# Kernel tuning notes

Measured on AMD Instinct MI355X. Metric: run time of the kernel, lower is better.

Reference implementation:

```python
import jax, jax.numpy as jnp
import numpy as np

B, D, K, M1, M2 = 256, 128, 32, 64, 32   # batch, n_nodes, K copies, dims[1], dims[2]
H1, H2, L = 128, 64, 32                   # pivae_dims


def setup_inputs() -> dict:
    key = jax.random.key(0)
    ks = iter(jax.random.split(key, 32))

    def rn(shape, scale):
        return jax.random.normal(next(ks), shape, dtype=jnp.float32) * scale

    x = jax.random.normal(next(ks), (B, D), dtype=jnp.float32)

    # per-node fc1 weights: [D, M1, D]; bounds force nonneg with zero diag column
    W1_pos = jnp.abs(rn((D, M1, D), 1.0 / np.sqrt(D)))
    W1_neg = jnp.abs(rn((D, M1, D), 1.0 / np.sqrt(D)))
    eye = jnp.eye(D, dtype=jnp.float32)[:, None, :]   # zero out W[j,:,j]
    W1_pos = W1_pos * (1.0 - eye)
    W1_neg = W1_neg * (1.0 - eye)
    b1_pos = rn((D, M1), 0.02)
    b1_neg = rn((D, M1), 0.02)

    # LocallyConnected stacks: weight [K, m_in, m_out]
    lc1_w = rn((K, M1, M2), 1.0 / np.sqrt(M1)); lc1_b = rn((K, M2), 0.02)
    lc2_w = rn((K, M2, 1), 1.0 / np.sqrt(M2));  lc2_b = rn((K, 1), 0.02)

    # per-sample beta Linear(k,1): weights [B, K], bias [B]
    beta_w = rn((B, K), 1.0 / np.sqrt(K)); beta_b = rn((B,), 0.02)

    # VAE params (encoder -> mu/logvar -> decoder), stored as (in,out) matrices
    enc1_w = rn((K, H1), 1.0 / np.sqrt(K));  enc1_b = jnp.zeros((H1,), jnp.float32)
    enc2_w = rn((H1, H2), 1.0 / np.sqrt(H1)); enc2_b = jnp.zeros((H2,), jnp.float32)
    mu_w = rn((H2, L), 1.0 / np.sqrt(H2));    mu_b = jnp.zeros((L,), jnp.float32)
    lv_w = rn((H2, L), 1.0 / np.sqrt(H2));    lv_b = jnp.zeros((L,), jnp.float32)
    dec1_w = rn((L, H2), 1.0 / np.sqrt(L));   dec1_b = jnp.zeros((H2,), jnp.float32)
    dec2_w = rn((H2, H1), 1.0 / np.sqrt(H2)); dec2_b = jnp.zeros((H1,), jnp.float32)
    dec3_w = rn((H1, K), 1.0 / np.sqrt(H1));  dec3_b = jnp.zeros((K,), jnp.float32)

    eps = jax.random.normal(next(ks), (B, L), dtype=jnp.float32)  # reparam noise

    return dict(x=x, W1_pos=W1_pos, W1_neg=W1_neg, b1_pos=b1_pos, b1_neg=b1_neg,
                lc1_w=lc1_w, lc1_b=lc1_b, lc2_w=lc2_w, lc2_b=lc2_b,
                beta_w=beta_w, beta_b=beta_b,
                enc1_w=enc1_w, enc1_b=enc1_b, enc2_w=enc2_w, enc2_b=enc2_b,
                mu_w=mu_w, mu_b=mu_b, lv_w=lv_w, lv_b=lv_b,
                dec1_w=dec1_w, dec1_b=dec1_b, dec2_w=dec2_w, dec2_b=dec2_b,
                dec3_w=dec3_w, dec3_b=dec3_b, eps=eps)


def reference(x, W1_pos, W1_neg, b1_pos, b1_neg, lc1_w, lc1_b, lc2_w, lc2_b,
              beta_w, beta_b, enc1_w, enc1_b, enc2_w, enc2_b, mu_w, mu_b,
              lv_w, lv_b, dec1_w, dec1_b, dec2_w, dec2_b, dec3_w, dec3_b, eps):
    b, d = x.shape
    k = lc1_w.shape[0]

    # fused per-node fc1: (pos - neg) applied to x with column j zeroed, all j at once
    W1 = W1_pos - W1_neg                      # [D, M1, D]
    b1 = b1_pos - b1_neg                      # [D, M1]
    full = jnp.einsum('bi,jhi->bjh', x, W1)   # as if no column were zeroed
    diagW = jnp.einsum('jhj->jh', W1)         # [D, M1] column-j weight of node j
    phi = full - x[:, :, None] * diagW[None] + b1[None]   # [B, D, M1]

    # expand to K copies, run sigmoid + LocallyConnected stack
    h = jnp.broadcast_to(phi[:, :, None, :], (b, d, k, phi.shape[-1]))
    h = jnp.einsum('bdkm,kmn->bdkn', jax.nn.sigmoid(h), lc1_w) + lc1_b   # [B,D,K,M2]
    h = jnp.einsum('bdkm,kmn->bdkn', jax.nn.sigmoid(h), lc2_w) + lc2_b   # [B,D,K,1]
    last_phi_x = h[..., 0]                    # [B, D, K]

    # per-sample beta projection (batched over B)
    y1 = jnp.einsum('bdk,bk->bd', last_phi_x, beta_w) + beta_b[:, None]

    # VAE on the stacked beta weights [B, K]
    e = jax.nn.relu(beta_w @ enc1_w + enc1_b)
    e = jax.nn.relu(e @ enc2_w + enc2_b)
    mu = e @ mu_w + mu_b
    logvar = e @ lv_w + lv_b
    z = mu + eps * jnp.exp(0.5 * logvar)
    dh = jax.nn.relu(z @ dec1_w + dec1_b)
    dh = jax.nn.relu(dh @ dec2_w + dec2_b)
    recon = dh @ dec3_w + dec3_b              # [B, K]

    y2 = jnp.einsum('bdk,bk->bd', last_phi_x, recon) + beta_b[:, None]
    return (y1, y2, mu, logvar)
```

## Files before the change

kernel.cpp:

```cpp
#include <hip/hip_runtime.h>
#include <stdint.h>

#define BB 256
#define DD 128
#define KK 32
#define MM1 64
#define MM2 32

typedef __attribute__((ext_vector_type(8))) short bf16x8;
typedef __attribute__((ext_vector_type(4))) float f32x4;

#define LOG2E 1.44269504088896f


__device__ __forceinline__ short f2b(float f) {
  uint32_t u = __builtin_bit_cast(uint32_t, f);
  u += 0x7FFFu + ((u >> 16) & 1u);
  return (short)(u >> 16);
}
__device__ __forceinline__ float sigm_pre(float acc, float cpre) {
  return __builtin_amdgcn_rcpf(
      1.0f + __builtin_amdgcn_exp2f(fmaf(acc, -LOG2E, cpre)));
}

__global__ __launch_bounds__(256) void prep_kernel(
    const float* __restrict__ x, const float* __restrict__ W1p,
    const float* __restrict__ W1n, const float* __restrict__ b1p,
    const float* __restrict__ b1n, const float* __restrict__ lc1w,
    const float* __restrict__ lc1b, const float* __restrict__ lc2b,
    const float* __restrict__ betaw, char* __restrict__ ws)
{
  const int tid = blockIdx.x * 256 + threadIdx.x;

  {
    float4 a = ((const float4*)W1p)[tid];
    float4 b = ((const float4*)W1n)[tid];
    short4 s;
    s.x = f2b(a.x - b.x); s.y = f2b(a.y - b.y);
    s.z = f2b(a.z - b.z); s.w = f2b(a.w - b.w);
    ((short4*)(ws + 303104))[tid] = s;
  }
  if (tid < 8192) {
    float4 v = ((const float4*)x)[tid];
    short4 s;
    s.x = f2b(v.x); s.y = f2b(v.y); s.z = f2b(v.z); s.w = f2b(v.w);
    ((short4*)(ws + 65536))[tid] = s;
  }
  if (tid < 65536) {
    int k = tid >> 11, n = (tid >> 6) & 31, m = tid & 63;
    ((short*)(ws + 131072))[tid] = f2b(lc1w[k * 2048 + m * 32 + n]);
  }
  if (tid < 8192) {
    ((float*)(ws + 32768))[tid] = betaw[(tid & 255) * 32 + (tid >> 8)];
  }
  if (tid < 1024) {
    ((float*)(ws + 262144))[tid] = -lc1b[tid] * LOG2E;
  }
  if (tid < 32) { ((float*)(ws + 266240))[tid] = 0.25f * lc2b[tid]; }
  if (tid < 8192) {
    ((float*)(ws + 270336))[tid] = -(b1p[tid] - b1n[tid]) * LOG2E;
  }
}

__global__ __launch_bounds__(128) void vae_kernel(
    const float* __restrict__ betaw,
    const float* __restrict__ enc1w, const float* __restrict__ enc1b,
    const float* __restrict__ enc2w, const float* __restrict__ enc2b,
    const float* __restrict__ muw,  const float* __restrict__ mub,
    const float* __restrict__ lvw,  const float* __restrict__ lvb,
    const float* __restrict__ dec1w, const float* __restrict__ dec1b,
    const float* __restrict__ dec2w, const float* __restrict__ dec2b,
    const float* __restrict__ dec3w, const float* __restrict__ dec3b,
    const float* __restrict__ eps,
    float* __restrict__ mu_out, float* __restrict__ lv_out,
    float* __restrict__ reconT)
{
  const int b = blockIdx.x, t = threadIdx.x;
  __shared__ float bw[KK], e1[128], e2[64], zz[32], d1s[64], d2s[128];
  if (t < KK) bw[t] = betaw[b * KK + t];
  __syncthreads();
  {
    float a0 = enc1b[t], a1 = 0.f;
    #pragma unroll
    for (int k = 0; k < KK; k += 2) {
      a0 = fmaf(bw[k], enc1w[k * 128 + t], a0);
      a1 = fmaf(bw[k + 1], enc1w[(k + 1) * 128 + t], a1);
    }
    e1[t] = fmaxf(a0 + a1, 0.f);
  }
  __syncthreads();
  if (t < 64) {
    float a0 = enc2b[t], a1 = 0.f, a2 = 0.f, a3 = 0.f;
    #pragma unroll 8
    for (int h = 0; h < 128; h += 4) {
      a0 = fmaf(e1[h], enc2w[h * 64 + t], a0);
      a1 = fmaf(e1[h + 1], enc2w[(h + 1) * 64 + t], a1);
      a2 = fmaf(e1[h + 2], enc2w[(h + 2) * 64 + t], a2);
      a3 = fmaf(e1[h + 3], enc2w[(h + 3) * 64 + t], a3);
    }
    e2[t] = fmaxf((a0 + a1) + (a2 + a3), 0.f);
  }
  __syncthreads();
  if (t < 32) {
    float m0 = mub[t], m1 = 0.f, l0 = lvb[t], l1 = 0.f;
    #pragma unroll 8
    for (int h = 0; h < 64; h += 2) {
      float ea = e2[h], eb = e2[h + 1];
      m0 = fmaf(ea, muw[h * 32 + t], m0);
      m1 = fmaf(eb, muw[(h + 1) * 32 + t], m1);
      l0 = fmaf(ea, lvw[h * 32 + t], l0);
      l1 = fmaf(eb, lvw[(h + 1) * 32 + t], l1);
    }
    float m = m0 + m1, l = l0 + l1;
    mu_out[b * 32 + t] = m;
    lv_out[b * 32 + t] = l;
    zz[t] = fmaf(eps[b * 32 + t], __expf(0.5f * l), m);
  }
  __syncthreads();
  if (t < 64) {
    float a0 = dec1b[t], a1 = 0.f;
    #pragma unroll
    for (int l = 0; l < 32; l += 2) {
      a0 = fmaf(zz[l], dec1w[l * 64 + t], a0);
      a1 = fmaf(zz[l + 1], dec1w[(l + 1) * 64 + t], a1);
    }
    d1s[t] = fmaxf(a0 + a1, 0.f);
  }
  __syncthreads();
  {
    float a0 = dec2b[t], a1 = 0.f, a2 = 0.f, a3 = 0.f;
    #pragma unroll 8
    for (int h = 0; h < 64; h += 4) {
      a0 = fmaf(d1s[h], dec2w[h * 128 + t], a0);
      a1 = fmaf(d1s[h + 1], dec2w[(h + 1) * 128 + t], a1);
      a2 = fmaf(d1s[h + 2], dec2w[(h + 2) * 128 + t], a2);
      a3 = fmaf(d1s[h + 3], dec2w[(h + 3) * 128 + t], a3);
    }
    d2s[t] = fmaxf((a0 + a1) + (a2 + a3), 0.f);
  }
  __syncthreads();
  if (t < 32) {
    float a0 = dec3b[t], a1 = 0.f, a2 = 0.f, a3 = 0.f;
    #pragma unroll 8
    for (int h = 0; h < 128; h += 4) {
      a0 = fmaf(d2s[h], dec3w[h * 32 + t], a0);
      a1 = fmaf(d2s[h + 1], dec3w[(h + 1) * 32 + t], a1);
      a2 = fmaf(d2s[h + 2], dec3w[(h + 2) * 32 + t], a2);
      a3 = fmaf(d2s[h + 3], dec3w[(h + 3) * 32 + t], a3);
    }
    reconT[t * BB + b] = (a0 + a1) + (a2 + a3);
  }
}

__global__ __launch_bounds__(256) void main_kernel(
    const float* __restrict__ lc2w, const float* __restrict__ betab,
    const char* __restrict__ ws, float* __restrict__ out)
{
  const int bx = blockIdx.x;
  const int d = bx >> 3;
  const int bg = bx & 7;
  const int tid = threadIdx.x;
  const int wave = tid >> 6, lane = tid & 63;
  const int g = lane >> 4, l15 = lane & 15;
  const int gb0 = bg * 32 + l15, gb1 = gb0 + 16;

  const short* __restrict__ xbf   = (const short*)(ws + 65536);
  const short* __restrict__ lc1T  = (const short*)(ws + 131072);
  const float* __restrict__ lc1bs = (const float*)(ws + 262144);
  const float* __restrict__ lc2bq = (const float*)(ws + 266240);
  const float* __restrict__ b1s   = (const float*)(ws + 270336) + d * MM1;
  const short* __restrict__ w1bf  = (const short*)(ws + 303104) + d * (MM1 * DD);
  const float* __restrict__ betaT = (const float*)(ws + 32768);
  const float* __restrict__ recT  = (const float*)(ws + 0);

  __shared__ short sS[32 * 64];
  __shared__ float yred[4][64];

  {
    bf16x8 wbv[4];
    const int m = wave * 16 + l15;
    #pragma unroll
    for (int ks = 0; ks < 4; ++ks)
      wbv[ks] = *(const bf16x8*)(w1bf + m * DD + ks * 32 + g * 8);
    const float cpre = b1s[m];
    #pragma unroll
    for (int rt = 0; rt < 2; ++rt) {
      f32x4 acc = {0.f, 0.f, 0.f, 0.f};
      #pragma unroll
      for (int ks = 0; ks < 4; ++ks) {
        bf16x8 xa = *(const bf16x8*)(xbf + (bg * 32 + rt * 16 + l15) * DD +
                                     ks * 32 + g * 8);
        acc = __builtin_amdgcn_mfma_f32_16x16x32_bf16(xa, wbv[ks], acc, 0, 0, 0);
      }
      #pragma unroll
      for (int r = 0; r < 4; ++r) {
        const int bl = rt * 16 + g * 4 + r;
        float s = sigm_pre(acc[r], cpre);
        sS[bl * 64 + ((m & ~7) ^ ((bl & 7) << 3)) + (m & 7)] = f2b(s);
      }
    }
  }
  __syncthreads();

  const bf16x8 sa0 = *(const bf16x8*)&sS[l15 * 64 + ((g * 8) ^ ((l15 & 7) << 3))];
  const bf16x8 sa1 = *(const bf16x8*)&sS[l15 * 64 + ((32 + g * 8) ^ ((l15 & 7) << 3))];
  const bf16x8 sa2 = *(const bf16x8*)&sS[(16 + l15) * 64 + ((g * 8) ^ ((l15 & 7) << 3))];
  const bf16x8 sa3 = *(const bf16x8*)&sS[(16 + l15) * 64 + ((32 + g * 8) ^ ((l15 & 7) << 3))];

  float y1a = 0.f, y2a = 0.f, y1b = 0.f, y2b = 0.f;
  bf16x8 A0a, A1a, A2a, A3a, A0b, A1b, A2b, A3b;

#define PREFA(kk, S) { \
    const short* ap = lc1T + (kk) * 2048 + l15 * 64 + g * 8; \
    A0##S = *(const bf16x8*)(ap); \
    A1##S = *(const bf16x8*)(ap + 32); \
    A2##S = *(const bf16x8*)(ap + 1024); \
    A3##S = *(const bf16x8*)(ap + 1056); }

#define COMPUTE(kk, S) { \
    f32x4 acc00 = {0,0,0,0}, acc01 = {0,0,0,0}; \
    f32x4 acc10 = {0,0,0,0}, acc11 = {0,0,0,0}; \
    acc00 = __builtin_amdgcn_mfma_f32_16x16x32_bf16(A0##S, sa0, acc00, 0, 0, 0); \
    acc00 = __builtin_amdgcn_mfma_f32_16x16x32_bf16(A1##S, sa1, acc00, 0, 0, 0); \
    acc01 = __builtin_amdgcn_mfma_f32_16x16x32_bf16(A0##S, sa2, acc01, 0, 0, 0); \
    acc01 = __builtin_amdgcn_mfma_f32_16x16x32_bf16(A1##S, sa3, acc01, 0, 0, 0); \
    acc10 = __builtin_amdgcn_mfma_f32_16x16x32_bf16(A2##S, sa0, acc10, 0, 0, 0); \
    acc10 = __builtin_amdgcn_mfma_f32_16x16x32_bf16(A3##S, sa1, acc10, 0, 0, 0); \
    acc11 = __builtin_amdgcn_mfma_f32_16x16x32_bf16(A2##S, sa2, acc11, 0, 0, 0); \
    acc11 = __builtin_amdgcn_mfma_f32_16x16x32_bf16(A3##S, sa3, acc11, 0, 0, 0); \
    f32x4 w0 = *(const f32x4*)(lc2w + (kk) * 32 + g * 4); \
    f32x4 w1 = *(const f32x4*)(lc2w + (kk) * 32 + 16 + g * 4); \
    f32x4 c0 = *(const f32x4*)(lc1bs + (kk) * 32 + g * 4); \
    f32x4 c1 = *(const f32x4*)(lc1bs + (kk) * 32 + 16 + g * 4); \
    float va = lc2bq[kk], vb = va; \
    _Pragma("unroll") \
    for (int r = 0; r < 4; ++r) { \
      va = fmaf(sigm_pre(acc00[r], c0[r]), w0[r], va); \
      va = fmaf(sigm_pre(acc10[r], c1[r]), w1[r], va); \
      vb = fmaf(sigm_pre(acc01[r], c0[r]), w0[r], vb); \
      vb = fmaf(sigm_pre(acc11[r], c1[r]), w1[r], vb); \
    } \
    y1a = fmaf(va, betaT[(kk) * BB + gb0], y1a); \
    y2a = fmaf(va, recT[(kk) * BB + gb0], y2a); \
    y1b = fmaf(vb, betaT[(kk) * BB + gb1], y1b); \
    y2b = fmaf(vb, recT[(kk) * BB + gb1], y2b); }

  const int k0 = wave * 8;
  PREFA(k0, a);
  #pragma unroll
  for (int kk = 0; kk < 8; kk += 2) {
    PREFA(k0 + kk + 1, b);
    COMPUTE(k0 + kk, a);
    if (kk < 6) PREFA(k0 + kk + 2, a);
    COMPUTE(k0 + kk + 1, b);
  }
#undef PREFA
#undef COMPUTE

  y1a += __shfl_xor(y1a, 16, 64); y1a += __shfl_xor(y1a, 32, 64);
  y2a += __shfl_xor(y2a, 16, 64); y2a += __shfl_xor(y2a, 32, 64);
  y1b += __shfl_xor(y1b, 16, 64); y1b += __shfl_xor(y1b, 32, 64);
  y2b += __shfl_xor(y2b, 16, 64); y2b += __shfl_xor(y2b, 32, 64);

  if (g == 0) {
    yred[wave][l15 * 2 + 0] = y1a;
    yred[wave][l15 * 2 + 1] = y2a;
    yred[wave][32 + l15 * 2 + 0] = y1b;
    yred[wave][32 + l15 * 2 + 1] = y2b;
  }
  __syncthreads();
  if (tid < 64) {
    float s = yred[0][tid] + yred[1][tid] + yred[2][tid] + yred[3][tid];
    const int rt = tid >> 5, q = tid & 31, l = q >> 1, o = q & 1;
    const int b = bg * 32 + rt * 16 + l;
    s += betab[b];
    out[o * (BB * DD) + b * DD + d] = s;
  }
}

extern "C" void kernel_launch(void* const* d_in, const int* in_sizes, int n_in,
                              void* d_out, int out_size, void* d_ws, size_t ws_size,
                              hipStream_t stream) {
  const float* x     = (const float*)d_in[0];
  const float* W1p   = (const float*)d_in[1];
  const float* W1n   = (const float*)d_in[2];
  const float* b1p   = (const float*)d_in[3];
  const float* b1n   = (const float*)d_in[4];
  const float* lc1w  = (const float*)d_in[5];
  const float* lc1b  = (const float*)d_in[6];
  const float* lc2w  = (const float*)d_in[7];
  const float* lc2b  = (const float*)d_in[8];
  const float* betaw = (const float*)d_in[9];
  const float* betab = (const float*)d_in[10];
  const float* enc1w = (const float*)d_in[11];
  const float* enc1b = (const float*)d_in[12];
  const float* enc2w = (const float*)d_in[13];
  const float* enc2b = (const float*)d_in[14];
  const float* muw   = (const float*)d_in[15];
  const float* mub   = (const float*)d_in[16];
  const float* lvw   = (const float*)d_in[17];
  const float* lvb   = (const float*)d_in[18];
  const float* dec1w = (const float*)d_in[19];
  const float* dec1b = (const float*)d_in[20];
  const float* dec2w = (const float*)d_in[21];
  const float* dec2b = (const float*)d_in[22];
  const float* dec3w = (const float*)d_in[23];
  const float* dec3b = (const float*)d_in[24];
  const float* eps   = (const float*)d_in[25];

  float* out    = (float*)d_out;
  char*  ws     = (char*)d_ws;
  float* reconT = (float*)ws;
  float* mu_out = out + BB * DD * 2;
  float* lv_out = mu_out + BB * 32;

  prep_kernel<<<dim3(1024), dim3(256), 0, stream>>>(
      x, W1p, W1n, b1p, b1n, lc1w, lc1b, lc2b, betaw, ws);

  vae_kernel<<<dim3(BB), dim3(128), 0, stream>>>(
      betaw, enc1w, enc1b, enc2w, enc2b, muw, mub, lvw, lvb,
      dec1w, dec1b, dec2w, dec2b, dec3w, dec3b, eps,
      mu_out, lv_out, reconT);

  main_kernel<<<dim3(1024), dim3(256), 0, stream>>>(
      lc2w, betab, (const char*)ws, out);
}
```

Measured before the change: 148.9 us.

## Merge prep and VAE kernels; retile main kernel to 64 batch rows per block

Folds the prep and VAE kernels into one launch, with extra blocks handling the VAE, so one kernel launch and a dependency gap disappear. The main kernel now uses 512-thread blocks covering 64 batch rows per node. Each wave keeps its four K-slices of the LC1 weights in registers and reuses them across four row tiles. The LC1 bias and LC2 weights are staged in shared memory. This cuts repeated global weight loads and halves the block count, in exchange for higher register pressure (launch bounds 512,4) and the loss of the earlier software prefetch pipeline.

After: 150.4 us. No clear change (+1.0%).

```diff
diff --git a/kernel.cpp b/kernel.cpp
--- a/kernel.cpp
+++ b/kernel.cpp
@@ -23,46 +23,11 @@
       1.0f + __builtin_amdgcn_exp2f(fmaf(acc, -LOG2E, cpre)));
 }
 
-__global__ __launch_bounds__(256) void prep_kernel(
+__global__ __launch_bounds__(256) void combo_kernel(
     const float* __restrict__ x, const float* __restrict__ W1p,
     const float* __restrict__ W1n, const float* __restrict__ b1p,
     const float* __restrict__ b1n, const float* __restrict__ lc1w,
     const float* __restrict__ lc1b, const float* __restrict__ lc2b,
-    const float* __restrict__ betaw, char* __restrict__ ws)
-{
-  const int tid = blockIdx.x * 256 + threadIdx.x;
-
-  {
-    float4 a = ((const float4*)W1p)[tid];
-    float4 b = ((const float4*)W1n)[tid];
-    short4 s;
-    s.x = f2b(a.x - b.x); s.y = f2b(a.y - b.y);
-    s.z = f2b(a.z - b.z); s.w = f2b(a.w - b.w);
-    ((short4*)(ws + 303104))[tid] = s;
-  }
-  if (tid < 8192) {
-    float4 v = ((const float4*)x)[tid];
-    short4 s;
-    s.x = f2b(v.x); s.y = f2b(v.y); s.z = f2b(v.z); s.w = f2b(v.w);
-    ((short4*)(ws + 65536))[tid] = s;
-  }
-  if (tid < 65536) {
-    int k = tid >> 11, n = (tid >> 6) & 31, m = tid & 63;
-    ((short*)(ws + 131072))[tid] = f2b(lc1w[k * 2048 + m * 32 + n]);
-  }
-  if (tid < 8192) {
-    ((float*)(ws + 32768))[tid] = betaw[(tid & 255) * 32 + (tid >> 8)];
-  }
-  if (tid < 1024) {
-    ((float*)(ws + 262144))[tid] = -lc1b[tid] * LOG2E;
-  }
-  if (tid < 32) { ((float*)(ws + 266240))[tid] = 0.25f * lc2b[tid]; }
-  if (tid < 8192) {
-    ((float*)(ws + 270336))[tid] = -(b1p[tid] - b1n[tid]) * LOG2E;
-  }
-}
-
-__global__ __launch_bounds__(128) void vae_kernel(
     const float* __restrict__ betaw,
     const float* __restrict__ enc1w, const float* __restrict__ enc1b,
     const float* __restrict__ enc2w, const float* __restrict__ enc2b,
@@ -72,14 +37,47 @@
     const float* __restrict__ dec2w, const float* __restrict__ dec2b,
     const float* __restrict__ dec3w, const float* __restrict__ dec3b,
     const float* __restrict__ eps,
-    float* __restrict__ mu_out, float* __restrict__ lv_out,
-    float* __restrict__ reconT)
+    char* __restrict__ ws, float* __restrict__ mu_out,
+    float* __restrict__ lv_out)
 {
-  const int b = blockIdx.x, t = threadIdx.x;
+  const int bx = blockIdx.x;
+  if (bx < 1024) {
+    const int tid = bx * 256 + threadIdx.x;
+    {
+      float4 a = ((const float4*)W1p)[tid];
+      float4 b = ((const float4*)W1n)[tid];
+      short4 s;
+      s.x = f2b(a.x - b.x); s.y = f2b(a.y - b.y);
+      s.z = f2b(a.z - b.z); s.w = f2b(a.w - b.w);
+      ((short4*)(ws + 303104))[tid] = s;
+    }
+    if (tid < 8192) {
+      float4 v = ((const float4*)x)[tid];
+      short4 s;
+      s.x = f2b(v.x); s.y = f2b(v.y); s.z = f2b(v.z); s.w = f2b(v.w);
+      ((short4*)(ws + 65536))[tid] = s;
+    }
+    if (tid < 65536) {
+      int k = tid >> 11, n = (tid >> 6) & 31, m = tid & 63;
+      ((short*)(ws + 131072))[tid] = f2b(lc1w[k * 2048 + m * 32 + n]);
+    }
+    if (tid < 8192) {
+      ((float*)(ws + 32768))[tid] = betaw[(tid & 255) * 32 + (tid >> 8)];
+    }
+    if (tid < 1024) { ((float*)(ws + 262144))[tid] = -lc1b[tid] * LOG2E; }
+    if (tid < 32) { ((float*)(ws + 266240))[tid] = 0.25f * lc2b[tid]; }
+    if (tid < 8192) {
+      ((float*)(ws + 270336))[tid] = -(b1p[tid] - b1n[tid]) * LOG2E;
+    }
+    return;
+  }
+
+  const int b = bx - 1024, t = threadIdx.x;
+  float* reconT = (float*)ws;
   __shared__ float bw[KK], e1[128], e2[64], zz[32], d1s[64], d2s[128];
   if (t < KK) bw[t] = betaw[b * KK + t];
   __syncthreads();
-  {
+  if (t < 128) {
     float a0 = enc1b[t], a1 = 0.f;
     #pragma unroll
     for (int k = 0; k < KK; k += 2) {
@@ -127,7 +125,7 @@
     d1s[t] = fmaxf(a0 + a1, 0.f);
   }
   __syncthreads();
-  {
+  if (t < 128) {
     float a0 = dec2b[t], a1 = 0.f, a2 = 0.f, a3 = 0.f;
     #pragma unroll 8
     for (int h = 0; h < 64; h += 4) {
@@ -152,17 +150,16 @@
   }
 }
 
-__global__ __launch_bounds__(256) void main_kernel(
+__global__ __launch_bounds__(512, 4) void main_kernel(
     const float* __restrict__ lc2w, const float* __restrict__ betab,
     const char* __restrict__ ws, float* __restrict__ out)
 {
   const int bx = blockIdx.x;
-  const int d = bx >> 3;
-  const int bg = bx & 7;
+  const int d = bx >> 2;
+  const int bh = bx & 3;
   const int tid = threadIdx.x;
   const int wave = tid >> 6, lane = tid & 63;
   const int g = lane >> 4, l15 = lane & 15;
-  const int gb0 = bg * 32 + l15, gb1 = gb0 + 16;
 
   const short* __restrict__ xbf   = (const short*)(ws + 65536);
   const short* __restrict__ lc1T  = (const short*)(ws + 131072);
@@ -173,108 +170,110 @@
   const float* __restrict__ betaT = (const float*)(ws + 32768);
   const float* __restrict__ recT  = (const float*)(ws + 0);
 
-  __shared__ short sS[32 * 64];
-  __shared__ float yred[4][64];
+  __shared__ __align__(16) short sS[64 * 64];
+  __shared__ __align__(16) float cS[1024];
+  __shared__ __align__(16) float wS[1024];
+  __shared__ float lbq[32];
+  __shared__ float yred[8][64][2];
+
+  if (tid < 256)      ((f32x4*)cS)[tid]       = ((const f32x4*)lc1bs)[tid];
+  else if (tid < 512) ((f32x4*)wS)[tid - 256] = ((const f32x4*)lc2w)[tid - 256];
+  if (tid < 32) lbq[tid] = lc2bq[tid];
+
+  bf16x8 Af[4][2][2];
+  #pragma unroll
+  for (int kk = 0; kk < 4; ++kk)
+    #pragma unroll
+    for (int nh = 0; nh < 2; ++nh)
+      #pragma unroll
+      for (int mh = 0; mh < 2; ++mh)
+        Af[kk][nh][mh] = *(const bf16x8*)(
+            lc1T + ((wave * 4 + kk) * 32 + nh * 16 + l15) * 64 + mh * 32 + g * 8);
 
   {
-    bf16x8 wbv[4];
-    const int m = wave * 16 + l15;
+    const int rt1 = wave >> 1, mt0 = (wave & 1) * 2;
+    bf16x8 xa[4];
     #pragma unroll
     for (int ks = 0; ks < 4; ++ks)
-      wbv[ks] = *(const bf16x8*)(w1bf + m * DD + ks * 32 + g * 8);
-    const float cpre = b1s[m];
-    #pragma unroll
-    for (int rt = 0; rt < 2; ++rt) {
+      xa[ks] = *(const bf16x8*)(
+          xbf + (bh * 64 + rt1 * 16 + l15) * DD + ks * 32 + g * 8);
+    #pragma unroll
+    for (int mi = 0; mi < 2; ++mi) {
+      const int m = (mt0 + mi) * 16 + l15;
       f32x4 acc = {0.f, 0.f, 0.f, 0.f};
       #pragma unroll
       for (int ks = 0; ks < 4; ++ks) {
-        bf16x8 xa = *(const bf16x8*)(xbf + (bg * 32 + rt * 16 + l15) * DD +
-                                     ks * 32 + g * 8);
-        acc = __builtin_amdgcn_mfma_f32_16x16x32_bf16(xa, wbv[ks], acc, 0, 0, 0);
+        bf16x8 wb = *(const bf16x8*)(w1bf + m * DD + ks * 32 + g * 8);
+        acc = __builtin_amdgcn_mfma_f32_16x16x32_bf16(xa[ks], wb, acc, 0, 0, 0);
       }
+      const float cpre = b1s[m];
       #pragma unroll
       for (int r = 0; r < 4; ++r) {
-        const int bl = rt * 16 + g * 4 + r;
-        float s = sigm_pre(acc[r], cpre);
-        sS[bl * 64 + ((m & ~7) ^ ((bl & 7) << 3)) + (m & 7)] = f2b(s);
+        const int bl = rt1 * 16 + g * 4 + r;
+        sS[bl * 64 + ((m & ~7) ^ ((bl & 7) << 3)) + (m & 7)] =
+            f2b(sigm_pre(acc[r], cpre));
       }
     }
   }
   __syncthreads();
 
-  const bf16x8 sa0 = *(const bf16x8*)&sS[l15 * 64 + ((g * 8) ^ ((l15 & 7) << 3))];
-  const bf16x8 sa1 = *(const bf16x8*)&sS[l15 * 64 + ((32 + g * 8) ^ ((l15 & 7) << 3))];
-  const bf16x8 sa2 = *(const bf16x8*)&sS[(16 + l15) * 64 + ((g * 8) ^ ((l15 & 7) << 3))];
-  const bf16x8 sa3 = *(const bf16x8*)&sS[(16 + l15) * 64 + ((32 + g * 8) ^ ((l15 & 7) << 3))];
-
-  float y1a = 0.f, y2a = 0.f, y1b = 0.f, y2b = 0.f;
-  bf16x8 A0a, A1a, A2a, A3a, A0b, A1b, A2b, A3b;
-
-#define PREFA(kk, S) { \
-    const short* ap = lc1T + (kk) * 2048 + l15 * 64 + g * 8; \
-    A0##S = *(const bf16x8*)(ap); \
-    A1##S = *(const bf16x8*)(ap + 32); \
-    A2##S = *(const bf16x8*)(ap + 1024); \
-    A3##S = *(const bf16x8*)(ap + 1056); }
-
-#define COMPUTE(kk, S) { \
-    f32x4 acc00 = {0,0,0,0}, acc01 = {0,0,0,0}; \
-    f32x4 acc10 = {0,0,0,0}, acc11 = {0,0,0,0}; \
-    acc00 = __builtin_amdgcn_mfma_f32_16x16x32_bf16(A0##S, sa0, acc00, 0, 0, 0); \
-    acc00 = __builtin_amdgcn_mfma_f32_16x16x32_bf16(A1##S, sa1, acc00, 0, 0, 0); \
-    acc01 = __builtin_amdgcn_mfma_f32_16x16x32_bf16(A0##S, sa2, acc01, 0, 0, 0); \
-    acc01 = __builtin_amdgcn_mfma_f32_16x16x32_bf16(A1##S, sa3, acc01, 0, 0, 0); \
-    acc10 = __builtin_amdgcn_mfma_f32_16x16x32_bf16(A2##S, sa0, acc10, 0, 0, 0); \
-    acc10 = __builtin_amdgcn_mfma_f32_16x16x32_bf16(A3##S, sa1, acc10, 0, 0, 0); \
-    acc11 = __builtin_amdgcn_mfma_f32_16x16x32_bf16(A2##S, sa2, acc11, 0, 0, 0); \
-    acc11 = __builtin_amdgcn_mfma_f32_16x16x32_bf16(A3##S, sa3, acc11, 0, 0, 0); \
-    f32x4 w0 = *(const f32x4*)(lc2w + (kk) * 32 + g * 4); \
-    f32x4 w1 = *(const f32x4*)(lc2w + (kk) * 32 + 16 + g * 4); \
-    f32x4 c0 = *(const f32x4*)(lc1bs + (kk) * 32 + g * 4); \
-    f32x4 c1 = *(const f32x4*)(lc1bs + (kk) * 32 + 16 + g * 4); \
-    float va = lc2bq[kk], vb = va; \
-    _Pragma("unroll") \
-    for (int r = 0; r < 4; ++r) { \
-      va = fmaf(sigm_pre(acc00[r], c0[r]), w0[r], va); \
-      va = fmaf(sigm_pre(acc10[r], c1[r]), w1[r], va); \
-      vb = fmaf(sigm_pre(acc01[r], c0[r]), w0[r], vb); \
-      vb = fmaf(sigm_pre(acc11[r], c1[r]), w1[r], vb); \
-    } \
-    y1a = fmaf(va, betaT[(kk) * BB + gb0], y1a); \
-    y2a = fmaf(va, recT[(kk) * BB + gb0], y2a); \
-    y1b = fmaf(vb, betaT[(kk) * BB + gb1], y1b); \
-    y2b = fmaf(vb, recT[(kk) * BB + gb1], y2b); }
-
-  const int k0 = wave * 8;
-  PREFA(k0, a);
+  float y1p[4] = {0, 0, 0, 0}, y2p[4] = {0, 0, 0, 0};
   #pragma unroll
-  for (int kk = 0; kk < 8; kk += 2) {
-    PREFA(k0 + kk + 1, b);
-    COMPUTE(k0 + kk, a);
-    if (kk < 6) PREFA(k0 + kk + 2, a);
-    COMPUTE(k0 + kk + 1, b);
-  }
-#undef PREFA
-#undef COMPUTE
-
-  y1a += __shfl_xor(y1a, 16, 64); y1a += __shfl_xor(y1a, 32, 64);
-  y2a += __shfl_xor(y2a, 16, 64); y2a += __shfl_xor(y2a, 32, 64);
-  y1b += __shfl_xor(y1b, 16, 64); y1b += __shfl_xor(y1b, 32, 64);
-  y2b += __shfl_xor(y2b, 16, 64); y2b += __shfl_xor(y2b, 32, 64);
-
+  for (int rt = 0; rt < 4; ++rt) {
+    const int b = rt * 16 + l15;
+    const int bsw = (b & 7) << 3;
+    const bf16x8 sa0 = *(const bf16x8*)&sS[b * 64 + ((g * 8) ^ bsw)];
+    const bf16x8 sa1 = *(const bf16x8*)&sS[b * 64 + ((32 + g * 8) ^ bsw)];
+    f32x4 acc[4][2];
+    #pragma unroll
+    for (int kk = 0; kk < 4; ++kk)
+      #pragma unroll
+      for (int nh = 0; nh < 2; ++nh) {
+        f32x4 a = {0.f, 0.f, 0.f, 0.f};
+        a = __builtin_amdgcn_mfma_f32_16x16x32_bf16(Af[kk][nh][0], sa0, a, 0, 0, 0);
+        a = __builtin_amdgcn_mfma_f32_16x16x32_bf16(Af[kk][nh][1], sa1, a, 0, 0, 0);
+        acc[kk][nh] = a;
+      }
+    const int gb = bh * 64 + b;
+    #pragma unroll
+    for (int kk = 0; kk < 4; ++kk) {
+      const int k = wave * 4 + kk;
+      float v = lbq[k];
+      #pragma unroll
+      for (int nh = 0; nh < 2; ++nh) {
+        const f32x4 c4 = *(const f32x4*)&cS[k * 32 + nh * 16 + g * 4];
+        const f32x4 w4 = *(const f32x4*)&wS[k * 32 + nh * 16 + g * 4];
+        #pragma unroll
+        for (int r = 0; r < 4; ++r)
+          v = fmaf(sigm_pre(acc[kk][nh][r], c4[r]), w4[r], v);
+      }
+      y1p[rt] = fmaf(v, betaT[k * BB + gb], y1p[rt]);
+      y2p[rt] = fmaf(v, recT[k * BB + gb], y2p[rt]);
+    }
+  }
+
+  #pragma unroll
+  for (int rt = 0; rt < 4; ++rt) {
+    y1p[rt] += __shfl_xor(y1p[rt], 16, 64);
+    y1p[rt] += __shfl_xor(y1p[rt], 32, 64);
+    y2p[rt] += __shfl_xor(y2p[rt], 16, 64);
+    y2p[rt] += __shfl_xor(y2p[rt], 32, 64);
+  }
   if (g == 0) {
-    yred[wave][l15 * 2 + 0] = y1a;
-    yred[wave][l15 * 2 + 1] = y2a;
-    yred[wave][32 + l15 * 2 + 0] = y1b;
-    yred[wave][32 + l15 * 2 + 1] = y2b;
-  }
-  __syncthreads();
-  if (tid < 64) {
-    float s = yred[0][tid] + yred[1][tid] + yred[2][tid] + yred[3][tid];
-    const int rt = tid >> 5, q = tid & 31, l = q >> 1, o = q & 1;
-    const int b = bg * 32 + rt * 16 + l;
-    s += betab[b];
-    out[o * (BB * DD) + b * DD + d] = s;
+    #pragma unroll
+    for (int rt = 0; rt < 4; ++rt) {
+      yred[wave][rt * 16 + l15][0] = y1p[rt];
+      yred[wave][rt * 16 + l15][1] = y2p[rt];
+    }
+  }
+  __syncthreads();
+  if (tid < 128) {
+    const int bl = tid >> 1, o = tid & 1;
+    float s = 0.f;
+    #pragma unroll
+    for (int w = 0; w < 8; ++w) s += yred[w][bl][o];
+    const int b = bh * 64 + bl;
+    out[o * (BB * DD) + b * DD + d] = s + betab[b];
   }
 }
 
@@ -310,18 +309,15 @@
 
   float* out    = (float*)d_out;
   char*  ws     = (char*)d_ws;
-  float* reconT = (float*)ws;
   float* mu_out = out + BB * DD * 2;
   float* lv_out = mu_out + BB * 32;
 
-  prep_kernel<<<dim3(1024), dim3(256), 0, stream>>>(
-      x, W1p, W1n, b1p, b1n, lc1w, lc1b, lc2b, betaw, ws);
-
-  vae_kernel<<<dim3(BB), dim3(128), 0, stream>>>(
-      betaw, enc1w, enc1b, enc2w, enc2b, muw, mub, lvw, lvb,
+  combo_kernel<<<dim3(1280), dim3(256), 0, stream>>>(
+      x, W1p, W1n, b1p, b1n, lc1w, lc1b, lc2b, betaw,
+      enc1w, enc1b, enc2w, enc2b, muw, mub, lvw, lvb,
       dec1w, dec1b, dec2w, dec2b, dec3w, dec3b, eps,
-      mu_out, lv_out, reconT);
-
-  main_kernel<<<dim3(1024), dim3(256), 0, stream>>>(
+      ws, mu_out, lv_out);
+
+  main_kernel<<<dim3(512), dim3(512), 0, stream>>>(
       lc2w, betab, (const char*)ws, out);
 }
```
